# Kernel optimization log

Measured on AMD Instinct MI355X. Metric: run time of the kernel, lower is better.

## Reference

```python
import jax, jax.numpy as jnp
import numpy as np

L, B, D = 2048, 2, 1024
H, DK, DV = 16, 64, 64
SPAN = 128
LN_EPS = 1e-5


def setup_inputs() -> dict:
    key = jax.random.key(0)
    ks = jax.random.split(key, 8)
    s_qk = np.sqrt(2.0 / (D + DK)).astype(np.float32)
    s_v = np.sqrt(2.0 / (D + DV)).astype(np.float32)
    return {
        "query": jax.random.normal(ks[0], (L, B, D), jnp.float32),
        "key": jax.random.normal(ks[1], (L, B, D), jnp.float32),
        "value": jax.random.normal(ks[2], (L, B, D), jnp.float32),
        "Wq": jax.random.normal(ks[3], (D, H * DK), jnp.float32) * s_qk,
        "bq": jnp.zeros((H * DK,), jnp.float32),
        "Wk": jax.random.normal(ks[4], (D, H * DK), jnp.float32) * s_qk,
        "bk": jnp.zeros((H * DK,), jnp.float32),
        "Wv": jax.random.normal(ks[5], (D, H * DV), jnp.float32) * s_v,
        "bv": jnp.zeros((H * DV,), jnp.float32),
        "Wfc": jax.random.normal(ks[6], (H * DV, D), jnp.float32) * np.sqrt(2.0 / (H * DV + D)).astype(np.float32),
        "bfc": jnp.zeros((D,), jnp.float32),
        "gamma": jnp.ones((D,), jnp.float32),
        "beta": jnp.zeros((D,), jnp.float32),
    }


def reference(query, key, value, Wq, bq, Wk, bk, Wv, bv, Wfc, bfc, gamma, beta):
    l, b, d = query.shape
    # projections: (l,b,H*dk) -> (H,b,l,dk)   [torch rearrange 'l b (head k) -> head b l k']
    q = (query @ Wq + bq).reshape(l, b, H, DK).transpose(2, 1, 0, 3)
    k = (key @ Wk + bk).reshape(l, b, H, DK).transpose(2, 1, 0, 3)
    v = (value @ Wv + bv).reshape(l, b, H, DV).transpose(2, 1, 0, 3)
    scores = jnp.einsum("hblk,hbtk->hblt", q, k) / jnp.sqrt(jnp.float32(DK))
    # banded additive mask: keep |j - i| <= SPAN
    idx = jnp.arange(l)
    band = jnp.abs(idx[None, :] - idx[:, None]) <= SPAN  # (l, l)
    scores = jnp.where(band[None, None], scores, -jnp.inf)
    attn = jax.nn.softmax(scores, axis=-1)
    out = jnp.einsum("hblt,hbtv->hblv", attn, v)
    # 'head b l v -> l b (head v)'
    out = out.transpose(2, 1, 0, 3).reshape(l, b, H * DV)
    out = out @ Wfc + bfc  # dropout p=0.0 -> identity
    y = out + query  # residual
    mu = jnp.mean(y, axis=-1, keepdims=True)
    var = jnp.mean(jnp.square(y - mu), axis=-1, keepdims=True)
    y = (y - mu) * jax.lax.rsqrt(var + LN_EPS) * gamma + beta
    return (y, attn)
```

## Files before the change

### kernel.cpp

```cpp
#include <hip/hip_runtime.h>
#include <stdint.h>

#define L_SEQ 2048
#define BB 2
#define DD 1024
#define NH 16
#define SPAN 128

typedef __attribute__((ext_vector_type(8))) short short8;
typedef __attribute__((ext_vector_type(4))) float floatx4;

__device__ __forceinline__ short f32_bf16(float f) {
  uint32_t u = __float_as_uint(f);
  u += 0x7FFFu + ((u >> 16) & 1u);
  return (short)(u >> 16);
}
__device__ __forceinline__ float bf2f(short s) {
  return __uint_as_float(((uint32_t)(uint16_t)s) << 16);
}

__device__ __forceinline__ void gld16(const short* g, short* l) {
  __builtin_amdgcn_global_load_lds(
      (__attribute__((address_space(1))) void*)(g),
      (__attribute__((address_space(3))) void*)(l), 16, 0, 0);
}

__global__ __launch_bounds__(256) void k_prep(
    const float* __restrict__ s0, const float* __restrict__ s1, const float* __restrict__ s2,
    const float* __restrict__ w0, const float* __restrict__ w1,
    const float* __restrict__ w2, const float* __restrict__ w3,
    short* __restrict__ d0, short* __restrict__ d1, short* __restrict__ d2,
    short* __restrict__ WT) {
  __shared__ float tile[64][65];
  int bid = blockIdx.x, tid = threadIdx.x;
  if (bid < 12288) {
    int y = bid >> 12;
    const float* s = y == 0 ? s0 : (y == 1 ? s1 : s2);
    short* d = y == 0 ? d0 : (y == 1 ? d1 : d2);
    int i = (bid & 4095) * 256 + tid;
    float4 v = ((const float4*)s)[i];
    short4 o;
    o.x = f32_bf16(v.x); o.y = f32_bf16(v.y); o.z = f32_bf16(v.z); o.w = f32_bf16(v.w);
    ((short4*)d)[i] = o;
  } else {
    int b2 = bid - 12288;
    int z = b2 >> 8;
    int xy = b2 & 255;
    int bx = (xy & 15) * 64, by = (xy >> 4) * 64;
    int tx = tid & 63, ty = tid >> 6;
    const float* src = z == 0 ? w0 : z == 1 ? w1 : z == 2 ? w2 : w3;
    short* out = WT + (size_t)z * (DD * DD);
#pragma unroll
    for (int r = 0; r < 64; r += 4)
      tile[ty + r][tx] = src[(size_t)(by + ty + r) * DD + bx + tx];
    __syncthreads();
    int r2 = tid >> 2, q = tid & 3;
    short8 o0, o1;
#pragma unroll
    for (int j = 0; j < 8; ++j) o0[j] = f32_bf16(tile[q * 16 + j][r2]);
#pragma unroll
    for (int j = 0; j < 8; ++j) o1[j] = f32_bf16(tile[q * 16 + 8 + j][r2]);
    *(short8*)(out + (size_t)(bx + r2) * DD + by + q * 16) = o0;
    *(short8*)(out + (size_t)(bx + r2) * DD + by + q * 16 + 8) = o1;
  }
}

#define BM 128
#define BN 128
#define SMEM_SH 17408

__device__ __forceinline__ void gemm_core(const short* __restrict__ A,
                                          const short* __restrict__ BT,
                                          floatx4 acc[4][4], int bm0, int bn0,
                                          short* smem) {
  int tid = threadIdx.x;
  int wave = tid >> 6, lane = tid & 63;
  int li = lane & 15, quad = lane >> 4;
  int wm = (wave & 1) * 64, wn = (wave >> 1) * 64;
  int r0 = wave * 32 + (lane >> 2);
  int c0 = (lane & 3) * 8;
  const short* gA = A + (size_t)(bm0 + r0) * DD + c0;
  const short* gB = BT + (size_t)(bn0 + r0) * DD + c0;
  short* sA = smem;
  short* sB = smem + 8192;
  {
    short* lA = sA + wave * 1024;
    short* lB = sB + wave * 1024;
    gld16(gA, lA);
    gld16(gA + (size_t)16 * DD, lA + 512);
    gld16(gB, lB);
    gld16(gB + (size_t)16 * DD, lB + 512);
  }
  __syncthreads();
#pragma unroll 2
  for (int k = 0; k < 32; ++k) {
    int cur = k & 1;
    if (k < 31) {
      int koff = (k + 1) * 32;
      short* lA = sA + (cur ^ 1) * 4096 + wave * 1024;
      short* lB = sB + (cur ^ 1) * 4096 + wave * 1024;
      gld16(gA + koff, lA);
      gld16(gA + (size_t)16 * DD + koff, lA + 512);
      gld16(gB + koff, lB);
      gld16(gB + (size_t)16 * DD + koff, lB + 512);
    }
    const short* cA = sA + cur * 4096;
    const short* cB = sB + cur * 4096;
    short8 af[4], bf[4];
#pragma unroll
    for (int t = 0; t < 4; ++t) {
      af[t] = *(const short8*)&cA[(wm + t * 16 + li) * 32 + quad * 8];
      bf[t] = *(const short8*)&cB[(wn + t * 16 + li) * 32 + quad * 8];
    }
#pragma unroll
    for (int tm = 0; tm < 4; ++tm)
#pragma unroll
      for (int tn = 0; tn < 4; ++tn)
        acc[tm][tn] = __builtin_amdgcn_mfma_f32_16x16x32_bf16(af[tm], bf[tn], acc[tm][tn], 0, 0, 0);
    __syncthreads();
  }
}

__global__ __launch_bounds__(256) void k_proj(
    const short* __restrict__ xq, const short* __restrict__ xk, const short* __restrict__ xv,
    const short* __restrict__ WT,
    const float* __restrict__ bq, const float* __restrict__ bk, const float* __restrict__ bv,
    short* __restrict__ qo, short* __restrict__ ko, short* __restrict__ vto) {
  __shared__ __attribute__((aligned(16))) short smem[SMEM_SH];
  int flat = (blockIdx.z * 32 + blockIdx.y) * 8 + blockIdx.x;
  int swz = (flat & 7) * 96 + (flat >> 3);
  int bxw = swz & 7, byw = (swz >> 3) & 31, mode = swz >> 8;
  const short* A = mode == 0 ? xq : (mode == 1 ? xk : xv);
  const short* BT = WT + (size_t)mode * DD * DD;
  const float* bias = mode == 0 ? bq : (mode == 1 ? bk : bv);
  floatx4 acc[4][4] = {};
  int bm0 = byw * BM, bn0 = bxw * BN;
  gemm_core(A, BT, acc, bm0, bn0, smem);

  int tid = threadIdx.x;
  int wave = tid >> 6, lane = tid & 63;
  int li = lane & 15, quad = lane >> 4;
  int wm = (wave & 1) * 64, wn = (wave >> 1) * 64;
#pragma unroll
  for (int tm = 0; tm < 4; ++tm)
#pragma unroll
    for (int tn = 0; tn < 4; ++tn) {
      int gn = bn0 + wn + tn * 16 + li;
      float bs = bias[gn];
#pragma unroll
      for (int r = 0; r < 4; ++r)
        smem[(wm + tm * 16 + quad * 4 + r) * 136 + wn + tn * 16 + li] =
            f32_bf16(acc[tm][tn][r] + bs);
    }
  __syncthreads();
  if (mode != 2) {
    short* dst = (mode == 0) ? qo : ko;
    int row = tid >> 1, half = tid & 1;
    int gm = bm0 + row, l = gm >> 1, b = gm & 1;
    int h = (bn0 + half * 64) >> 6;
    short* drow = dst + (((size_t)h * BB + b) * L_SEQ + l) * 64;
#pragma unroll
    for (int j = 0; j < 8; ++j)
      *(short8*)(drow + j * 8) = *(const short8*)&smem[row * 136 + half * 64 + j * 8];
  } else {
    int col = tid & 127, b2 = tid >> 7;
    int h2 = (bn0 + col) >> 6, dv = (bn0 + col) & 63;
    int l0 = bm0 >> 1;
    short* drow = vto + (((size_t)h2 * BB + b2) * 64 + dv) * L_SEQ + l0;
#pragma unroll
    for (int u0 = 0; u0 < 64; u0 += 8) {
      short8 o;
#pragma unroll
      for (int j = 0; j < 8; ++j)
        o[j] = smem[(2 * (u0 + j) + b2) * 136 + col];
      *(short8*)(drow + u0) = o;
    }
  }
}

__global__ __launch_bounds__(256) void k_attn(
    const short* __restrict__ qw, const short* __restrict__ kw, const short* __restrict__ vTw,
    float* __restrict__ attn_out, short* __restrict__ ctx) {
  __shared__ short sbuf[20480];
  short* K0 = sbuf;
  short* K1 = sbuf + 10240;
  const int tid = threadIdx.x;
  const int wv = tid >> 6, lane = tid & 63;
  const int li = lane & 15, quad = lane >> 4;
  int flat = blockIdx.y * 32 + blockIdx.x;
  int swz = (flat & 7) * 128 + (flat >> 3);
  const int i0b = (swz & 31) * 64;
  const int hb = swz >> 5;
  const int i0 = i0b + wv * 16;
  const int jb = i0b - SPAN;
  const short* Q = qw + (size_t)hb * L_SEQ * 64;
  const short* K = kw + (size_t)hb * L_SEQ * 64;
  const short* VT = vTw + (size_t)hb * 64 * L_SEQ;
  float* Aout = attn_out + (size_t)hb * L_SEQ * L_SEQ;

#pragma unroll
  for (int t = 0; t < 10; ++t) {
    int idx = wv + 4 * t;
    int half = idx >= 20 ? 1 : 0;
    int ridx = idx - half * 20;
    int row = ridx * 16 + (lane >> 2);
    int jr = jb + row;
    int jc = jr < 0 ? 0 : (jr >= L_SEQ ? L_SEQ - 1 : jr);
    const short* g = K + (size_t)jc * 64 + half * 32 + (lane & 3) * 8;
    short* l = (half ? K1 : K0) + ridx * 16 * 32;
    gld16(g, l);
  }

  short8 qf0 = *(const short8*)(Q + (size_t)(i0 + li) * 64 + quad * 8);
  short8 qf1 = *(const short8*)(Q + (size_t)(i0 + li) * 64 + 32 + quad * 8);
  __syncthreads();

  floatx4 S[17];
  const int jbase = i0 - SPAN;
  __builtin_amdgcn_s_setprio(1);
#pragma unroll
  for (int t = 0; t < 17; ++t) {
    int j0 = jbase + t * 16;
    floatx4 acc = {0.f, 0.f, 0.f, 0.f};
    if (j0 > -16 && j0 < L_SEQ) {
      int jrel = (wv + t) * 16;
      short8 kf0 = *(const short8*)&K0[(jrel + li) * 32 + quad * 8];
      short8 kf1 = *(const short8*)&K1[(jrel + li) * 32 + quad * 8];
      acc = __builtin_amdgcn_mfma_f32_16x16x32_bf16(qf0, kf0, acc, 0, 0, 0);
      acc = __builtin_amdgcn_mfma_f32_16x16x32_bf16(qf1, kf1, acc, 0, 0, 0);
    }
    S[t] = acc;
  }
  __builtin_amdgcn_s_setprio(0);
  float mrow[4] = {-1e30f, -1e30f, -1e30f, -1e30f};
#pragma unroll
  for (int t = 0; t < 17; ++t) {
    int j = jbase + t * 16 + li;
#pragma unroll
    for (int r = 0; r < 4; ++r) {
      int i = i0 + quad * 4 + r;
      bool inband = (j >= i - SPAN) && (j <= i + SPAN) && (j >= 0) && (j < L_SEQ);
      float s = inband ? S[t][r] * 0.125f : -1e30f;
      S[t][r] = s;
      mrow[r] = fmaxf(mrow[r], s);
    }
  }
#pragma unroll
  for (int m = 1; m <= 8; m <<= 1)
#pragma unroll
    for (int r = 0; r < 4; ++r) mrow[r] = fmaxf(mrow[r], __shfl_xor(mrow[r], m));
  float lsum[4] = {0.f, 0.f, 0.f, 0.f};
#pragma unroll
  for (int t = 0; t < 17; ++t)
#pragma unroll
    for (int r = 0; r < 4; ++r) {
      float p = __expf(S[t][r] - mrow[r]);
      S[t][r] = p;
      lsum[r] += p;
    }
#pragma unroll
  for (int m = 1; m <= 8; m <<= 1)
#pragma unroll
    for (int r = 0; r < 4; ++r) lsum[r] += __shfl_xor(lsum[r], m);
  float inv[4];
#pragma unroll
  for (int r = 0; r < 4; ++r) inv[r] = 1.0f / lsum[r];

  __syncthreads();
  short* myP = sbuf + wv * 4736;
#pragma unroll
  for (int t = 0; t < 17; ++t)
#pragma unroll
    for (int r = 0; r < 4; ++r)
      myP[(quad * 4 + r) * 296 + t * 16 + li] = f32_bf16(S[t][r] * inv[r]);
  *(short4*)&myP[(lane >> 2) * 296 + 272 + (lane & 3) * 4] = short4{0, 0, 0, 0};
  __syncthreads();

  floatx4 O[4] = {};
#pragma unroll
  for (int c = 0; c < 9; ++c) {
    short8 pf = *(const short8*)&myP[li * 296 + c * 32 + quad * 8];
    int jg = jbase + c * 32 + quad * 8;
    int jc = (jg >= 0 && jg < L_SEQ) ? jg : 0;
    short8 vf[4];
#pragma unroll
    for (int n = 0; n < 4; ++n)
      vf[n] = *(const short8*)(VT + (size_t)(n * 16 + li) * L_SEQ + jc);
    if (c < 8) {
#pragma unroll
      for (int rr = 0; rr < 2; ++rr) {
        int row = c * 2 + rr;
        float* orow = Aout + (size_t)(i0 + row) * L_SEQ;
        const short* prow = &myP[row * 296];
#pragma unroll
        for (int it = 0; it < 8; ++it) {
          int col = it * 256 + lane * 4;
          int s = col - jbase;
          floatx4 v = {0.f, 0.f, 0.f, 0.f};
          if (s >= 0 && s < 288) {
            short4 p4 = *(const short4*)(prow + s);
            v.x = bf2f(p4.x); v.y = bf2f(p4.y); v.z = bf2f(p4.z); v.w = bf2f(p4.w);
          }
          __builtin_nontemporal_store(v, (floatx4*)(orow + col));
        }
      }
    }
#pragma unroll
    for (int n = 0; n < 4; ++n)
      O[n] = __builtin_amdgcn_mfma_f32_16x16x32_bf16(pf, vf[n], O[n], 0, 0, 0);
  }
  const int b = hb & 1, h = hb >> 1;
#pragma unroll
  for (int n = 0; n < 4; ++n)
#pragma unroll
    for (int r = 0; r < 4; ++r) {
      int irow = quad * 4 + r;
      ctx[((size_t)(i0 + irow) * BB + b) * DD + h * 64 + n * 16 + li] = f32_bf16(O[n][r]);
    }
}

__global__ __launch_bounds__(256) void k_fc(
    const short* __restrict__ ctx, const short* __restrict__ WfcT,
    const float* __restrict__ bfc, const float* __restrict__ query,
    float* __restrict__ ypre) {
  __shared__ __attribute__((aligned(16))) short smem[SMEM_SH];
  int flat = blockIdx.y * 8 + blockIdx.x;
  int swz = (flat & 7) * 32 + (flat >> 3);
  int bm0 = (swz >> 3) * BM, bn0 = (swz & 7) * BN;
  floatx4 acc[4][4] = {};
  gemm_core(ctx, WfcT, acc, bm0, bn0, smem);
  int tid = threadIdx.x;
  int wave = tid >> 6, lane = tid & 63;
  int li = lane & 15, quad = lane >> 4;
  int wn = (wave >> 1) * 64;
  float* ft = (float*)smem;
#pragma unroll
  for (int hrow = 0; hrow < 2; ++hrow) {
    __syncthreads();
    if ((wave & 1) == hrow) {
#pragma unroll
      for (int tm = 0; tm < 4; ++tm)
#pragma unroll
        for (int tn = 0; tn < 4; ++tn) {
          int gn = bn0 + wn + tn * 16 + li;
          float bs = bfc[gn];
#pragma unroll
          for (int r = 0; r < 4; ++r)
            ft[(tm * 16 + quad * 4 + r) * 136 + wn + tn * 16 + li] = acc[tm][tn][r] + bs;
        }
    }
    __syncthreads();
    int row = tid >> 2, c0 = (tid & 3) * 32;
    int gm = bm0 + hrow * 64 + row;
    const float4* q4 = (const float4*)(query + (size_t)gm * DD + bn0 + c0);
    float4* o4 = (float4*)(ypre + (size_t)gm * DD + bn0 + c0);
#pragma unroll
    for (int v = 0; v < 8; ++v) {
      float4 a = *(const float4*)&ft[row * 136 + c0 + v * 4];
      float4 qq = q4[v];
      float4 o;
      o.x = a.x + qq.x; o.y = a.y + qq.y; o.z = a.z + qq.z; o.w = a.w + qq.w;
      o4[v] = o;
    }
  }
}

__global__ __launch_bounds__(256) void k_ln(
    const float* __restrict__ yp, const float* __restrict__ gamma,
    const float* __restrict__ beta, float* __restrict__ out) {
  __shared__ float red[8];
  int row = blockIdx.x, tid = threadIdx.x;
  float4 v = ((const float4*)(yp + (size_t)row * DD))[tid];
  float s = v.x + v.y + v.z + v.w;
  float s2 = v.x * v.x + v.y * v.y + v.z * v.z + v.w * v.w;
#pragma unroll
  for (int m = 1; m <= 32; m <<= 1) {
    s += __shfl_xor(s, m);
    s2 += __shfl_xor(s2, m);
  }
  int wv = tid >> 6;
  if ((tid & 63) == 0) { red[wv] = s; red[wv + 4] = s2; }
  __syncthreads();
  s = red[0] + red[1] + red[2] + red[3];
  s2 = red[4] + red[5] + red[6] + red[7];
  float mu = s * (1.0f / DD);
  float var = s2 * (1.0f / DD) - mu * mu;
  float rs = rsqrtf(var + 1e-5f);
  float4 g = ((const float4*)gamma)[tid];
  float4 bb = ((const float4*)beta)[tid];
  float4 o;
  o.x = (v.x - mu) * rs * g.x + bb.x;
  o.y = (v.y - mu) * rs * g.y + bb.y;
  o.z = (v.z - mu) * rs * g.z + bb.z;
  o.w = (v.w - mu) * rs * g.w + bb.w;
  ((float4*)(out + (size_t)row * DD))[tid] = o;
}

extern "C" void kernel_launch(void* const* d_in, const int* in_sizes, int n_in,
                              void* d_out, int out_size, void* d_ws, size_t ws_size,
                              hipStream_t stream) {
  const float* query = (const float*)d_in[0];
  const float* key   = (const float*)d_in[1];
  const float* value = (const float*)d_in[2];
  const float* Wq    = (const float*)d_in[3];
  const float* bq    = (const float*)d_in[4];
  const float* Wk    = (const float*)d_in[5];
  const float* bk    = (const float*)d_in[6];
  const float* Wv    = (const float*)d_in[7];
  const float* bv    = (const float*)d_in[8];
  const float* Wfc   = (const float*)d_in[9];
  const float* bfc   = (const float*)d_in[10];
  const float* gamma = (const float*)d_in[11];
  const float* beta  = (const float*)d_in[12];
  float* out = (float*)d_out;
  float* attn = out + (size_t)L_SEQ * BB * DD;

  char* w = (char*)d_ws;
  short* xq_b  = (short*)(w);
  short* xk_b  = (short*)(w + ((size_t)8 << 20));
  short* xv_b  = (short*)(w + ((size_t)16 << 20));
  short* WT    = (short*)(w + ((size_t)24 << 20));
  short* q_ws  = (short*)(w + ((size_t)32 << 20));
  short* k_ws  = (short*)(w + ((size_t)40 << 20));
  short* vT_ws = (short*)(w + ((size_t)56 << 20));
  short* ctx   = (short*)(w + ((size_t)64 << 20));
  float* ypre  = (float*)(w + ((size_t)72 << 20));

  k_prep<<<13312, 256, 0, stream>>>(query, key, value, Wq, Wk, Wv, Wfc,
                                    xq_b, xk_b, xv_b, WT);
  k_proj<<<dim3(8, 32, 3), 256, 0, stream>>>(xq_b, xk_b, xv_b, WT, bq, bk, bv, q_ws, k_ws, vT_ws);
  k_attn<<<dim3(32, 32), 256, 0, stream>>>(q_ws, k_ws, vT_ws, attn, ctx);
  k_fc<<<dim3(8, 32), 256, 0, stream>>>(ctx, WT + (size_t)3 * DD * DD, bfc, query, ypre);
  k_ln<<<4096, 256, 0, stream>>>(ypre, gamma, beta, out);
}
```

Baseline: 693.4 us.

## Distribute off-band attention zero-fill across projection, FC and layernorm kernels

Moves the zero stores for the out-of-band parts of the attention probability matrix out of the attention kernel and into the projection, output-FC and layernorm kernels. For the first sixteen head-batch slices the attention kernel now writes only the 256-column tiles overlapping the band. The aim is to hide the large zero-fill write traffic behind compute-heavy GEMM kernels and shorten the bandwidth-bound attention kernel. It relies on kernel ordering for correctness and adds store traffic to the other kernels.

```diff
diff --git a/kernel.cpp b/kernel.cpp
--- a/kernel.cpp
+++ b/kernel.cpp
@@ -23,6 +23,13 @@
   __builtin_amdgcn_global_load_lds(
       (__attribute__((address_space(1))) void*)(g),
       (__attribute__((address_space(3))) void*)(l), 16, 0, 0);
+}
+
+__device__ __forceinline__ void band_tiles(int i, int& itlo, int& ithi) {
+  int jbase = (i & ~15) - SPAN;
+  int lo = jbase < 0 ? 0 : jbase;
+  int hi = jbase + 287; if (hi > L_SEQ - 1) hi = L_SEQ - 1;
+  itlo = lo >> 8; ithi = hi >> 8;
 }
 
 __global__ __launch_bounds__(256) void k_prep(
@@ -125,7 +132,8 @@
     const short* __restrict__ xq, const short* __restrict__ xk, const short* __restrict__ xv,
     const short* __restrict__ WT,
     const float* __restrict__ bq, const float* __restrict__ bk, const float* __restrict__ bv,
-    short* __restrict__ qo, short* __restrict__ ko, short* __restrict__ vto) {
+    short* __restrict__ qo, short* __restrict__ ko, short* __restrict__ vto,
+    float* __restrict__ attn) {
   __shared__ __attribute__((aligned(16))) short smem[SMEM_SH];
   int flat = (blockIdx.z * 32 + blockIdx.y) * 8 + blockIdx.x;
   int swz = (flat & 7) * 96 + (flat >> 3);
@@ -175,6 +183,13 @@
         o[j] = smem[(2 * (u0 + j) + b2) * 136 + col];
       *(short8*)(drow + u0) = o;
     }
+  }
+  {
+    float* zb = attn + (size_t)flat * 65536 + tid * 4;
+    floatx4 zv = {0.f, 0.f, 0.f, 0.f};
+#pragma unroll
+    for (int j = 0; j < 64; ++j)
+      __builtin_nontemporal_store(zv, (floatx4*)(zb + j * 1024));
   }
 }
 
@@ -213,10 +228,16 @@
 
   short8 qf0 = *(const short8*)(Q + (size_t)(i0 + li) * 64 + quad * 8);
   short8 qf1 = *(const short8*)(Q + (size_t)(i0 + li) * 64 + 32 + quad * 8);
+
+  const int jbase = i0 - SPAN;
+  int itlo, ithi;
+  band_tiles(i0, itlo, ithi);
+  const int tlo = hb < 16 ? itlo : 0;
+  const int thi = hb < 16 ? ithi : 7;
+
   __syncthreads();
 
   floatx4 S[17];
-  const int jbase = i0 - SPAN;
   __builtin_amdgcn_s_setprio(1);
 #pragma unroll
   for (int t = 0; t < 17; ++t) {
@@ -292,8 +313,7 @@
         int row = c * 2 + rr;
         float* orow = Aout + (size_t)(i0 + row) * L_SEQ;
         const short* prow = &myP[row * 296];
-#pragma unroll
-        for (int it = 0; it < 8; ++it) {
+        for (int it = tlo; it <= thi; ++it) {
           int col = it * 256 + lane * 4;
           int s = col - jbase;
           floatx4 v = {0.f, 0.f, 0.f, 0.f};
@@ -322,7 +342,7 @@
 __global__ __launch_bounds__(256) void k_fc(
     const short* __restrict__ ctx, const short* __restrict__ WfcT,
     const float* __restrict__ bfc, const float* __restrict__ query,
-    float* __restrict__ ypre) {
+    float* __restrict__ ypre, float* __restrict__ attn) {
   __shared__ __attribute__((aligned(16))) short smem[SMEM_SH];
   int flat = blockIdx.y * 8 + blockIdx.x;
   int swz = (flat & 7) * 32 + (flat >> 3);
@@ -363,11 +383,27 @@
       o4[v] = o;
     }
   }
+  {
+    int base_row = flat * 24;
+    floatx4 zv = {0.f, 0.f, 0.f, 0.f};
+#pragma unroll
+    for (int rr = 0; rr < 6; ++rr) {
+      int R = base_row + wave + rr * 4;
+      int i = R & 2047;
+      int itlo, ithi;
+      band_tiles(i, itlo, ithi);
+      float* rowp = attn + ((size_t)(24576 + R)) * L_SEQ + lane * 4;
+      for (int it = 0; it < 8; ++it)
+        if (it < itlo || it > ithi)
+          __builtin_nontemporal_store(zv, (floatx4*)(rowp + it * 256));
+    }
+  }
 }
 
 __global__ __launch_bounds__(256) void k_ln(
     const float* __restrict__ yp, const float* __restrict__ gamma,
-    const float* __restrict__ beta, float* __restrict__ out) {
+    const float* __restrict__ beta, float* __restrict__ out,
+    float* __restrict__ attn) {
   __shared__ float red[8];
   int row = blockIdx.x, tid = threadIdx.x;
   float4 v = ((const float4*)(yp + (size_t)row * DD))[tid];
@@ -394,6 +430,17 @@
   o.z = (v.z - mu) * rs * g.z + bb.z;
   o.w = (v.w - mu) * rs * g.w + bb.w;
   ((float4*)(out + (size_t)row * DD))[tid] = o;
+  {
+    int i = blockIdx.x >> 1, halfsel = blockIdx.x & 1;
+    int itlo, ithi;
+    band_tiles(i, itlo, ithi);
+    int it = halfsel * 4 + wv;
+    if (it < itlo || it > ithi) {
+      floatx4 zv = {0.f, 0.f, 0.f, 0.f};
+      float* p = attn + ((size_t)(30720 + i)) * L_SEQ + it * 256 + (tid & 63) * 4;
+      __builtin_nontemporal_store(zv, (floatx4*)p);
+    }
+  }
 }
 
 extern "C" void kernel_launch(void* const* d_in, const int* in_sizes, int n_in,
@@ -428,8 +475,9 @@
 
   k_prep<<<13312, 256, 0, stream>>>(query, key, value, Wq, Wk, Wv, Wfc,
                                     xq_b, xk_b, xv_b, WT);
-  k_proj<<<dim3(8, 32, 3), 256, 0, stream>>>(xq_b, xk_b, xv_b, WT, bq, bk, bv, q_ws, k_ws, vT_ws);
+  k_proj<<<dim3(8, 32, 3), 256, 0, stream>>>(xq_b, xk_b, xv_b, WT, bq, bk, bv,
+                                             q_ws, k_ws, vT_ws, attn);
   k_attn<<<dim3(32, 32), 256, 0, stream>>>(q_ws, k_ws, vT_ws, attn, ctx);
-  k_fc<<<dim3(8, 32), 256, 0, stream>>>(ctx, WT + (size_t)3 * DD * DD, bfc, query, ypre);
-  k_ln<<<4096, 256, 0, stream>>>(ypre, gamma, beta, out);
-}
+  k_fc<<<dim3(8, 32), 256, 0, stream>>>(ctx, WT + (size_t)3 * DD * DD, bfc, query, ypre, attn);
+  k_ln<<<4096, 256, 0, stream>>>(ypre, gamma, beta, out, attn);
+}
```

Result: no change. 704.6 us (+1.6%).

## Store pre-LayerNorm activations as bf16 and coarsen the input conversion blocks

Applied to the files above, without the earlier changes.

The fc epilogue now adds bias and the residual query directly in registers and writes the pre-LayerNorm sum as bf16 through shared memory with wide stores. This replaces the two-pass fp32 staging, and LayerNorm reads bf16 instead of fp32, halving that intermediate traffic. The input fp32-to-bf16 conversion also gives each thread 8 float4 elements instead of one, which cuts the block count. Rounding the residual sum to bf16 before LayerNorm lowers output precision, and the residual query is now read per element in a strided pattern rather than coalesced.

```diff
diff --git a/kernel.cpp b/kernel.cpp
--- a/kernel.cpp
+++ b/kernel.cpp
@@ -33,17 +33,20 @@
     short* __restrict__ WT) {
   __shared__ float tile[64][65];
   int bid = blockIdx.x, tid = threadIdx.x;
-  if (bid < 12288) {
-    int y = bid >> 12;
+  if (bid < 1536) {
+    int y = bid >> 9;
     const float* s = y == 0 ? s0 : (y == 1 ? s1 : s2);
     short* d = y == 0 ? d0 : (y == 1 ? d1 : d2);
-    int i = (bid & 4095) * 256 + tid;
-    float4 v = ((const float4*)s)[i];
-    short4 o;
-    o.x = f32_bf16(v.x); o.y = f32_bf16(v.y); o.z = f32_bf16(v.z); o.w = f32_bf16(v.w);
-    ((short4*)d)[i] = o;
+    int i = (bid & 511) * 2048 + tid * 8;
+#pragma unroll
+    for (int j = 0; j < 8; ++j) {
+      float4 v = ((const float4*)s)[i + j];
+      short4 o;
+      o.x = f32_bf16(v.x); o.y = f32_bf16(v.y); o.z = f32_bf16(v.z); o.w = f32_bf16(v.w);
+      ((short4*)d)[i + j] = o;
+    }
   } else {
-    int b2 = bid - 12288;
+    int b2 = bid - 1536;
     int z = b2 >> 8;
     int xy = b2 & 255;
     int bx = (xy & 15) * 64, by = (xy >> 4) * 64;
@@ -322,7 +325,7 @@
 __global__ __launch_bounds__(256) void k_fc(
     const short* __restrict__ ctx, const short* __restrict__ WfcT,
     const float* __restrict__ bfc, const float* __restrict__ query,
-    float* __restrict__ ypre) {
+    short* __restrict__ ypre) {
   __shared__ __attribute__((aligned(16))) short smem[SMEM_SH];
   int flat = blockIdx.y * 8 + blockIdx.x;
   int swz = (flat & 7) * 32 + (flat >> 3);
@@ -332,45 +335,37 @@
   int tid = threadIdx.x;
   int wave = tid >> 6, lane = tid & 63;
   int li = lane & 15, quad = lane >> 4;
-  int wn = (wave >> 1) * 64;
-  float* ft = (float*)smem;
-#pragma unroll
-  for (int hrow = 0; hrow < 2; ++hrow) {
-    __syncthreads();
-    if ((wave & 1) == hrow) {
-#pragma unroll
-      for (int tm = 0; tm < 4; ++tm)
-#pragma unroll
-        for (int tn = 0; tn < 4; ++tn) {
-          int gn = bn0 + wn + tn * 16 + li;
-          float bs = bfc[gn];
-#pragma unroll
-          for (int r = 0; r < 4; ++r)
-            ft[(tm * 16 + quad * 4 + r) * 136 + wn + tn * 16 + li] = acc[tm][tn][r] + bs;
-        }
-    }
-    __syncthreads();
-    int row = tid >> 2, c0 = (tid & 3) * 32;
-    int gm = bm0 + hrow * 64 + row;
-    const float4* q4 = (const float4*)(query + (size_t)gm * DD + bn0 + c0);
-    float4* o4 = (float4*)(ypre + (size_t)gm * DD + bn0 + c0);
-#pragma unroll
-    for (int v = 0; v < 8; ++v) {
-      float4 a = *(const float4*)&ft[row * 136 + c0 + v * 4];
-      float4 qq = q4[v];
-      float4 o;
-      o.x = a.x + qq.x; o.y = a.y + qq.y; o.z = a.z + qq.z; o.w = a.w + qq.w;
-      o4[v] = o;
-    }
-  }
+  int wm = (wave & 1) * 64, wn = (wave >> 1) * 64;
+#pragma unroll
+  for (int tm = 0; tm < 4; ++tm)
+#pragma unroll
+    for (int tn = 0; tn < 4; ++tn) {
+      int gn = bn0 + wn + tn * 16 + li;
+      float bs = bfc[gn];
+#pragma unroll
+      for (int r = 0; r < 4; ++r) {
+        int gm = bm0 + wm + tm * 16 + quad * 4 + r;
+        smem[(wm + tm * 16 + quad * 4 + r) * 136 + wn + tn * 16 + li] =
+            f32_bf16(acc[tm][tn][r] + bs + query[(size_t)gm * DD + gn]);
+      }
+    }
+  __syncthreads();
+  int row = tid >> 1, half = tid & 1;
+  int gm = bm0 + row;
+  short* drow = ypre + (size_t)gm * DD + bn0 + half * 64;
+#pragma unroll
+  for (int j = 0; j < 8; ++j)
+    *(short8*)(drow + j * 8) = *(const short8*)&smem[row * 136 + half * 64 + j * 8];
 }
 
 __global__ __launch_bounds__(256) void k_ln(
-    const float* __restrict__ yp, const float* __restrict__ gamma,
+    const short* __restrict__ yp, const float* __restrict__ gamma,
     const float* __restrict__ beta, float* __restrict__ out) {
   __shared__ float red[8];
   int row = blockIdx.x, tid = threadIdx.x;
-  float4 v = ((const float4*)(yp + (size_t)row * DD))[tid];
+  short4 h4 = ((const short4*)(yp + (size_t)row * DD))[tid];
+  float4 v;
+  v.x = bf2f(h4.x); v.y = bf2f(h4.y); v.z = bf2f(h4.z); v.w = bf2f(h4.w);
   float s = v.x + v.y + v.z + v.w;
   float s2 = v.x * v.x + v.y * v.y + v.z * v.z + v.w * v.w;
 #pragma unroll
@@ -424,10 +419,10 @@
   short* k_ws  = (short*)(w + ((size_t)40 << 20));
   short* vT_ws = (short*)(w + ((size_t)56 << 20));
   short* ctx   = (short*)(w + ((size_t)64 << 20));
-  float* ypre  = (float*)(w + ((size_t)72 << 20));
-
-  k_prep<<<13312, 256, 0, stream>>>(query, key, value, Wq, Wk, Wv, Wfc,
-                                    xq_b, xk_b, xv_b, WT);
+  short* ypre  = (short*)(w + ((size_t)72 << 20));
+
+  k_prep<<<2560, 256, 0, stream>>>(query, key, value, Wq, Wk, Wv, Wfc,
+                                   xq_b, xk_b, xv_b, WT);
   k_proj<<<dim3(8, 32, 3), 256, 0, stream>>>(xq_b, xk_b, xv_b, WT, bq, bk, bv, q_ws, k_ws, vT_ws);
   k_attn<<<dim3(32, 32), 256, 0, stream>>>(q_ws, k_ws, vT_ws, attn, ctx);
   k_fc<<<dim3(8, 32), 256, 0, stream>>>(ctx, WT + (size_t)3 * DD * DD, bfc, query, ypre);
```

Result: no change. 689.5 us (-0.6%).
